# Kernel tuning notes

Measured on AMD Instinct MI355X. Metric: run time of the kernel, lower is better.

The kernel has to match this reference:

```python
import jax, jax.numpy as jnp
import numpy as np
import math

D_MODEL = 1024
NUM_HEADS = 16
D_K = D_MODEL // NUM_HEADS
B, L = 2, 2048


def setup_inputs() -> dict:
    key = jax.random.key(0)
    ks = jax.random.split(key, 9)
    s = 1.0 / math.sqrt(D_MODEL)
    inp = {
        "x": jax.random.normal(ks[0], (B, L, D_MODEL), dtype=jnp.float32),
        "mask": jnp.ones((B, L), dtype=jnp.int32),
        "Wq": jax.random.uniform(ks[1], (D_MODEL, D_MODEL), jnp.float32, -s, s),
        "bq": jax.random.uniform(ks[2], (D_MODEL,), jnp.float32, -s, s),
        "Wk": jax.random.uniform(ks[3], (D_MODEL, D_MODEL), jnp.float32, -s, s),
        "bk": jax.random.uniform(ks[4], (D_MODEL,), jnp.float32, -s, s),
        "Wv": jax.random.uniform(ks[5], (D_MODEL, D_MODEL), jnp.float32, -s, s),
        "bv": jax.random.uniform(ks[6], (D_MODEL,), jnp.float32, -s, s),
        "Wo": jax.random.uniform(ks[7], (D_MODEL, D_MODEL), jnp.float32, -s, s),
        "bo": jax.random.uniform(ks[8], (D_MODEL,), jnp.float32, -s, s),
    }
    return inp


def reference(x, mask, Wq, bq, Wk, bk, Wv, bv, Wo, bo):
    b, l, _ = x.shape
    def proj(W, bias):
        # nn.Linear: x @ W.T + b, then split heads -> [B, H, L, d_k]
        y = x @ W.T + bias
        return y.reshape(b, l, NUM_HEADS, D_K).transpose(0, 2, 1, 3)
    Q, K, V = proj(Wq, bq), proj(Wk, bk), proj(Wv, bv)
    scores = jnp.einsum("bhqd,bhkd->bhqk", Q, K) / math.sqrt(D_K)
    # mask: [B, L] -> [B, 1, 1, L]; fill masked positions with -1e9
    m = mask[:, None, None, :]
    scores = jnp.where(m == 0, jnp.float32(-1e9), scores)
    attn = jax.nn.softmax(scores, axis=-1)
    out = jnp.einsum("bhqk,bhkd->bhqd", attn, V)
    out = out.transpose(0, 2, 1, 3).reshape(b, l, D_MODEL)
    return out @ Wo.T + bo, attn
```

## Files before the change

kernel.cpp:

```cpp
#include <hip/hip_runtime.h>

#define D_MODEL 1024
#define NHEADS  16
#define DKH     64
#define BATCH   2
#define SEQ     2048
#define MTOT    (BATCH*SEQ)
#define NQKV    (3*D_MODEL)
#define LDT     72

typedef __bf16 bf16x8 __attribute__((ext_vector_type(8)));
typedef float  f32x4  __attribute__((ext_vector_type(4)));
typedef unsigned short u16x8 __attribute__((ext_vector_type(8)));
typedef unsigned short u16x4 __attribute__((ext_vector_type(4)));

#define MFMA(a,b,c) __builtin_amdgcn_mfma_f32_16x16x32_bf16(a,b,c,0,0,0)

__device__ __forceinline__ unsigned short f2bf(float f) {
  unsigned u = __builtin_bit_cast(unsigned, f);
  u += 0x7fffu + ((u >> 16) & 1u);
  return (unsigned short)(u >> 16);
}

__device__ __forceinline__ bf16x8 ldfrag(const unsigned short* p) {
  return __builtin_bit_cast(bf16x8, *(const u16x8*)p);
}

__global__ __launch_bounds__(256) void cvt_kernel(const float* __restrict__ src,
                                                  unsigned short* __restrict__ dst, int n4) {
  int i = blockIdx.x * blockDim.x + threadIdx.x;
  if (i >= n4) return;
  float4 f = ((const float4*)src)[i];
  u16x4 o;
  o[0] = f2bf(f.x); o[1] = f2bf(f.y); o[2] = f2bf(f.z); o[3] = f2bf(f.w);
  ((u16x4*)dst)[i] = o;
}

__global__ __launch_bounds__(256) void qkv_gemm(const unsigned short* __restrict__ xbf,
                                                const unsigned short* __restrict__ wbf,
                                                const float* __restrict__ bq,
                                                const float* __restrict__ bk,
                                                const float* __restrict__ bv,
                                                unsigned short* __restrict__ Qo,
                                                unsigned short* __restrict__ Ko,
                                                unsigned short* __restrict__ VTo)
{
  __shared__ __attribute__((aligned(16))) unsigned short As[64*LDT];
  __shared__ __attribute__((aligned(16))) unsigned short Bs[64*LDT];
  const int tid  = threadIdx.x;
  const int wid  = tid >> 6;
  const int lane = tid & 63;
  const int lr   = lane & 15;
  const int lg   = lane >> 4;
  const int m0   = blockIdx.x * 64;
  const int n0   = blockIdx.y * 64;

  f32x4 zero = {0.f, 0.f, 0.f, 0.f};
  f32x4 acc[4];
  acc[0] = zero; acc[1] = zero; acc[2] = zero; acc[3] = zero;

  const int ko = lg * 8;
  for (int kt = 0; kt < D_MODEL/64; ++kt) {
    __syncthreads();
    for (int v = tid; v < 512; v += 256) {
      int row = v >> 3, c8 = (v & 7) * 8;
      *(u16x8*)&As[row*LDT + c8] = *(const u16x8*)&xbf[(size_t)(m0+row)*D_MODEL + kt*64 + c8];
      *(u16x8*)&Bs[row*LDT + c8] = *(const u16x8*)&wbf[(size_t)(n0+row)*D_MODEL + kt*64 + c8];
    }
    __syncthreads();
    bf16x8 a0 = ldfrag(&As[(wid*16+lr)*LDT + ko]);
    bf16x8 a1 = ldfrag(&As[(wid*16+lr)*LDT + 32 + ko]);
#pragma unroll
    for (int ct = 0; ct < 4; ++ct) {
      bf16x8 b0 = ldfrag(&Bs[(ct*16+lr)*LDT + ko]);
      bf16x8 b1 = ldfrag(&Bs[(ct*16+lr)*LDT + 32 + ko]);
      acc[ct] = MFMA(a0, b0, acc[ct]);
      acc[ct] = MFMA(a1, b1, acc[ct]);
    }
  }

  const int proj = n0 >> 10;
  const int rem0 = n0 & 1023;
  const int h    = rem0 >> 6;
  const float* bias = (proj == 0) ? bq : (proj == 1) ? bk : bv;

  if (proj < 2) {
    unsigned short* dst = (proj == 0) ? Qo : Ko;
#pragma unroll
    for (int ct = 0; ct < 4; ++ct) {
      int col = ct*16 + lr;
      float bval = bias[rem0 + col];
#pragma unroll
      for (int r = 0; r < 4; ++r) {
        int m  = m0 + wid*16 + lg*4 + r;
        int b_ = m >> 11, lq = m & (SEQ-1);
        dst[((size_t)((b_*NHEADS + h)*SEQ + lq))*DKH + col] = f2bf(acc[ct][r] + bval);
      }
    }
  } else {
    __syncthreads();
#pragma unroll
    for (int ct = 0; ct < 4; ++ct) {
      int col = ct*16 + lr;
      float bval = bias[rem0 + col];
#pragma unroll
      for (int r = 0; r < 4; ++r) {
        int row = wid*16 + lg*4 + r;
        As[col*LDT + row] = f2bf(acc[ct][r] + bval);
      }
    }
    __syncthreads();
    int b_ = m0 >> 11, lq0 = m0 & (SEQ-1);
    int bh = b_*NHEADS + h;
    for (int v = tid; v < 512; v += 256) {
      int dk = v >> 3, c8 = (v & 7) * 8;
      *(u16x8*)&VTo[((size_t)(bh*DKH + dk))*SEQ + lq0 + c8] = *(const u16x8*)&As[dk*LDT + c8];
    }
  }
}

__global__ __launch_bounds__(256) void attn_kernel(const unsigned short* __restrict__ Qw,
                                                   const unsigned short* __restrict__ Kw,
                                                   const unsigned short* __restrict__ VTw,
                                                   const int* __restrict__ mask,
                                                   float* __restrict__ attn_out,
                                                   unsigned short* __restrict__ OH)
{
  __shared__ __attribute__((aligned(16))) unsigned short Qs[64*LDT];
  __shared__ __attribute__((aligned(16))) unsigned short Ks[64*LDT];
  __shared__ __attribute__((aligned(16))) unsigned short Vs[64*LDT];
  __shared__ __attribute__((aligned(16))) unsigned short Ps[64*LDT];
  __shared__ float invl[64];

  const int tid  = threadIdx.x;
  const int wid  = tid >> 6;
  const int lane = tid & 63;
  const int lr   = lane & 15;
  const int lg   = lane >> 4;
  const int q0   = blockIdx.x * 64;
  const int bh   = blockIdx.y;
  const int b_   = bh >> 4;
  const int h    = bh & 15;

  const unsigned short* Qb = Qw  + (size_t)bh*SEQ*DKH;
  const unsigned short* Kb = Kw  + (size_t)bh*SEQ*DKH;
  const unsigned short* Vb = VTw + (size_t)bh*DKH*SEQ;

  for (int v = tid; v < 512; v += 256) {
    int row = v >> 3, c8 = (v & 7) * 8;
    *(u16x8*)&Qs[row*LDT + c8] = *(const u16x8*)&Qb[(size_t)(q0+row)*DKH + c8];
  }
  __syncthreads();

  const int ko = lg * 8;
  bf16x8 aq0 = ldfrag(&Qs[(wid*16+lr)*LDT + ko]);
  bf16x8 aq1 = ldfrag(&Qs[(wid*16+lr)*LDT + 32 + ko]);

  f32x4 zero = {0.f, 0.f, 0.f, 0.f};
  float lsum[4] = {0.f, 0.f, 0.f, 0.f};

  for (int kt = 0; kt < SEQ/64; ++kt) {
    __syncthreads();
    for (int v = tid; v < 512; v += 256) {
      int row = v >> 3, c8 = (v & 7) * 8;
      *(u16x8*)&Ks[row*LDT + c8] = *(const u16x8*)&Kb[(size_t)(kt*64+row)*DKH + c8];
    }
    __syncthreads();
#pragma unroll
    for (int ct = 0; ct < 4; ++ct) {
      f32x4 acc = zero;
      bf16x8 b0 = ldfrag(&Ks[(ct*16+lr)*LDT + ko]);
      bf16x8 b1 = ldfrag(&Ks[(ct*16+lr)*LDT + 32 + ko]);
      acc = MFMA(aq0, b0, acc);
      acc = MFMA(aq1, b1, acc);
      int kg = kt*64 + ct*16 + lr;
      bool live = mask[b_*SEQ + kg] != 0;
#pragma unroll
      for (int r = 0; r < 4; ++r) {
        float s = live ? acc[r]*0.125f : -1e9f;
        lsum[r] += __expf(s);
      }
    }
  }
#pragma unroll
  for (int r = 0; r < 4; ++r) {
    float s = lsum[r];
    s += __shfl_xor(s, 1); s += __shfl_xor(s, 2);
    s += __shfl_xor(s, 4); s += __shfl_xor(s, 8);
    if (lr == 0) invl[wid*16 + lg*4 + r] = 1.0f / s;
  }
  __syncthreads();

  float il[4];
  {
    int rowb = wid*16 + lg*4;
    il[0] = invl[rowb+0]; il[1] = invl[rowb+1];
    il[2] = invl[rowb+2]; il[3] = invl[rowb+3];
  }

  f32x4 oacc[4];
  oacc[0] = zero; oacc[1] = zero; oacc[2] = zero; oacc[3] = zero;

  for (int kt = 0; kt < SEQ/64; ++kt) {
    __syncthreads();
    for (int v = tid; v < 512; v += 256) {
      int row = v >> 3, c8 = (v & 7) * 8;
      *(u16x8*)&Ks[row*LDT + c8] = *(const u16x8*)&Kb[(size_t)(kt*64+row)*DKH + c8];
      *(u16x8*)&Vs[row*LDT + c8] = *(const u16x8*)&Vb[(size_t)row*SEQ + kt*64 + c8];
    }
    __syncthreads();
#pragma unroll
    for (int ct = 0; ct < 4; ++ct) {
      f32x4 acc = zero;
      bf16x8 b0 = ldfrag(&Ks[(ct*16+lr)*LDT + ko]);
      bf16x8 b1 = ldfrag(&Ks[(ct*16+lr)*LDT + 32 + ko]);
      acc = MFMA(aq0, b0, acc);
      acc = MFMA(aq1, b1, acc);
      int kg = kt*64 + ct*16 + lr;
      bool live = mask[b_*SEQ + kg] != 0;
#pragma unroll
      for (int r = 0; r < 4; ++r) {
        float s = live ? acc[r]*0.125f : -1e9f;
        float p = __expf(s);
        int row = wid*16 + lg*4 + r;
        float a = p * il[r];
        attn_out[(size_t)(bh*SEQ + q0 + row)*SEQ + kg] = a;
        Ps[row*LDT + ct*16 + lr] = f2bf(a);
      }
    }
    __syncthreads();
    bf16x8 pa0 = ldfrag(&Ps[(wid*16+lr)*LDT + ko]);
    bf16x8 pa1 = ldfrag(&Ps[(wid*16+lr)*LDT + 32 + ko]);
#pragma unroll
    for (int ct = 0; ct < 4; ++ct) {
      bf16x8 v0 = ldfrag(&Vs[(ct*16+lr)*LDT + ko]);
      bf16x8 v1 = ldfrag(&Vs[(ct*16+lr)*LDT + 32 + ko]);
      oacc[ct] = MFMA(pa0, v0, oacc[ct]);
      oacc[ct] = MFMA(pa1, v1, oacc[ct]);
    }
  }

#pragma unroll
  for (int ct = 0; ct < 4; ++ct) {
    int dk = ct*16 + lr;
#pragma unroll
    for (int r = 0; r < 4; ++r) {
      int q = q0 + wid*16 + lg*4 + r;
      OH[(size_t)(b_*SEQ + q)*D_MODEL + h*DKH + dk] = f2bf(oacc[ct][r]);
    }
  }
}

__global__ __launch_bounds__(256) void out_gemm(const unsigned short* __restrict__ OH,
                                                const unsigned short* __restrict__ wo,
                                                const float* __restrict__ bo,
                                                float* __restrict__ out)
{
  __shared__ __attribute__((aligned(16))) unsigned short As[64*LDT];
  __shared__ __attribute__((aligned(16))) unsigned short Bs[64*LDT];
  const int tid  = threadIdx.x;
  const int wid  = tid >> 6;
  const int lane = tid & 63;
  const int lr   = lane & 15;
  const int lg   = lane >> 4;
  const int m0   = blockIdx.x * 64;
  const int n0   = blockIdx.y * 64;

  f32x4 zero = {0.f, 0.f, 0.f, 0.f};
  f32x4 acc[4];
  acc[0] = zero; acc[1] = zero; acc[2] = zero; acc[3] = zero;

  const int ko = lg * 8;
  for (int kt = 0; kt < D_MODEL/64; ++kt) {
    __syncthreads();
    for (int v = tid; v < 512; v += 256) {
      int row = v >> 3, c8 = (v & 7) * 8;
      *(u16x8*)&As[row*LDT + c8] = *(const u16x8*)&OH[(size_t)(m0+row)*D_MODEL + kt*64 + c8];
      *(u16x8*)&Bs[row*LDT + c8] = *(const u16x8*)&wo[(size_t)(n0+row)*D_MODEL + kt*64 + c8];
    }
    __syncthreads();
    bf16x8 a0 = ldfrag(&As[(wid*16+lr)*LDT + ko]);
    bf16x8 a1 = ldfrag(&As[(wid*16+lr)*LDT + 32 + ko]);
#pragma unroll
    for (int ct = 0; ct < 4; ++ct) {
      bf16x8 b0 = ldfrag(&Bs[(ct*16+lr)*LDT + ko]);
      bf16x8 b1 = ldfrag(&Bs[(ct*16+lr)*LDT + 32 + ko]);
      acc[ct] = MFMA(a0, b0, acc[ct]);
      acc[ct] = MFMA(a1, b1, acc[ct]);
    }
  }
#pragma unroll
  for (int ct = 0; ct < 4; ++ct) {
    int n = n0 + ct*16 + lr;
    float bval = bo[n];
#pragma unroll
    for (int r = 0; r < 4; ++r) {
      int m = m0 + wid*16 + lg*4 + r;
      out[(size_t)m*D_MODEL + n] = acc[ct][r] + bval;
    }
  }
}

extern "C" void kernel_launch(void* const* d_in, const int* in_sizes, int n_in,
                              void* d_out, int out_size, void* d_ws, size_t ws_size,
                              hipStream_t stream) {
  const float* x    = (const float*)d_in[0];
  const int*   mask = (const int*)  d_in[1];
  const float* Wq   = (const float*)d_in[2];
  const float* bq   = (const float*)d_in[3];
  const float* Wk   = (const float*)d_in[4];
  const float* bk   = (const float*)d_in[5];
  const float* Wv   = (const float*)d_in[6];
  const float* bv   = (const float*)d_in[7];
  const float* Wo   = (const float*)d_in[8];
  const float* bo   = (const float*)d_in[9];

  float* out0 = (float*)d_out;
  float* attn = out0 + (size_t)MTOT * D_MODEL;

  unsigned short* ws   = (unsigned short*)d_ws;
  unsigned short* xbf  = ws;
  unsigned short* wqkv = xbf  + (size_t)MTOT * D_MODEL;
  unsigned short* wob  = wqkv + (size_t)NQKV * D_MODEL;
  unsigned short* Qw   = wob  + (size_t)D_MODEL * D_MODEL;
  unsigned short* Kw   = Qw   + (size_t)MTOT * D_MODEL;
  unsigned short* VTw  = Kw   + (size_t)MTOT * D_MODEL;
  unsigned short* OH   = VTw  + (size_t)MTOT * D_MODEL;

  cvt_kernel<<<4096, 256, 0, stream>>>(x,  xbf, MTOT*D_MODEL/4);
  cvt_kernel<<<1024, 256, 0, stream>>>(Wq, wqkv,                 D_MODEL*D_MODEL/4);
  cvt_kernel<<<1024, 256, 0, stream>>>(Wk, wqkv +   D_MODEL*D_MODEL, D_MODEL*D_MODEL/4);
  cvt_kernel<<<1024, 256, 0, stream>>>(Wv, wqkv + 2*D_MODEL*D_MODEL, D_MODEL*D_MODEL/4);
  cvt_kernel<<<1024, 256, 0, stream>>>(Wo, wob, D_MODEL*D_MODEL/4);

  qkv_gemm<<<dim3(MTOT/64, NQKV/64), 256, 0, stream>>>(xbf, wqkv, bq, bk, bv, Qw, Kw, VTw);
  attn_kernel<<<dim3(SEQ/64, BATCH*NHEADS), 256, 0, stream>>>(Qw, Kw, VTw, mask, attn, OH);
  out_gemm<<<dim3(MTOT/64, D_MODEL/64), 256, 0, stream>>>(OH, wob, bo, out0);
}
```

Before: 821.3 us.

## Transpose score MFMA, drop LDS K/V staging, precompute additive mask, vectorize attn stores

Swaps the MFMA operand order so each lane owns one query row. K, Q and V^T fragments are now loaded straight from global memory instead of being staged in shared memory, which removes all block-wide barriers from both passes. The mask is precomputed once into an additive float buffer placed in the reused x workspace, and the 1/sqrt(dk) scale is folded into an exp2 argument. Attention probabilities are written as non-temporal float4 stores, and P is staged in a per-wave shared tile. The risk is more redundant global and L2 traffic for K/V, since each wave fetches its own fragments with no shared-memory reuse.

```diff
diff --git a/kernel.cpp b/kernel.cpp
--- a/kernel.cpp
+++ b/kernel.cpp
@@ -8,6 +8,7 @@
 #define MTOT    (BATCH*SEQ)
 #define NQKV    (3*D_MODEL)
 #define LDT     72
+#define LDP     72
 
 typedef __bf16 bf16x8 __attribute__((ext_vector_type(8)));
 typedef float  f32x4  __attribute__((ext_vector_type(4)));
@@ -15,6 +16,12 @@
 typedef unsigned short u16x4 __attribute__((ext_vector_type(4)));
 
 #define MFMA(a,b,c) __builtin_amdgcn_mfma_f32_16x16x32_bf16(a,b,c,0,0,0)
+
+#if __has_builtin(__builtin_amdgcn_exp2f)
+#define EXP2(x) __builtin_amdgcn_exp2f(x)
+#else
+#define EXP2(x) exp2f(x)
+#endif
 
 __device__ __forceinline__ unsigned short f2bf(float f) {
   unsigned u = __builtin_bit_cast(unsigned, f);
@@ -34,6 +41,12 @@
   u16x4 o;
   o[0] = f2bf(f.x); o[1] = f2bf(f.y); o[2] = f2bf(f.z); o[3] = f2bf(f.w);
   ((u16x4*)dst)[i] = o;
+}
+
+__global__ __launch_bounds__(256) void mask_kernel(const int* __restrict__ m,
+                                                   float* __restrict__ mf, int n) {
+  int i = blockIdx.x * blockDim.x + threadIdx.x;
+  if (i < n) mf[i] = m[i] ? 0.0f : -1e9f;
 }
 
 __global__ __launch_bounds__(256) void qkv_gemm(const unsigned short* __restrict__ xbf,
@@ -122,15 +135,11 @@
 __global__ __launch_bounds__(256) void attn_kernel(const unsigned short* __restrict__ Qw,
                                                    const unsigned short* __restrict__ Kw,
                                                    const unsigned short* __restrict__ VTw,
-                                                   const int* __restrict__ mask,
+                                                   const float* __restrict__ maskf,
                                                    float* __restrict__ attn_out,
                                                    unsigned short* __restrict__ OH)
 {
-  __shared__ __attribute__((aligned(16))) unsigned short Qs[64*LDT];
-  __shared__ __attribute__((aligned(16))) unsigned short Ks[64*LDT];
-  __shared__ __attribute__((aligned(16))) unsigned short Vs[64*LDT];
-  __shared__ __attribute__((aligned(16))) unsigned short Ps[64*LDT];
-  __shared__ float invl[64];
+  __shared__ __attribute__((aligned(16))) unsigned short Ps[4*16*LDP];
 
   const int tid  = threadIdx.x;
   const int wid  = tid >> 6;
@@ -145,96 +154,71 @@
   const unsigned short* Qb = Qw  + (size_t)bh*SEQ*DKH;
   const unsigned short* Kb = Kw  + (size_t)bh*SEQ*DKH;
   const unsigned short* Vb = VTw + (size_t)bh*DKH*SEQ;
-
-  for (int v = tid; v < 512; v += 256) {
-    int row = v >> 3, c8 = (v & 7) * 8;
-    *(u16x8*)&Qs[row*LDT + c8] = *(const u16x8*)&Qb[(size_t)(q0+row)*DKH + c8];
-  }
-  __syncthreads();
-
-  const int ko = lg * 8;
-  bf16x8 aq0 = ldfrag(&Qs[(wid*16+lr)*LDT + ko]);
-  bf16x8 aq1 = ldfrag(&Qs[(wid*16+lr)*LDT + 32 + ko]);
-
+  const f32x4* mf4 = (const f32x4*)(maskf + b_*SEQ);
+
+  const int qrow = q0 + wid*16 + lr;
+  bf16x8 aq0 = ldfrag(&Qb[(size_t)qrow*DKH + lg*8]);
+  bf16x8 aq1 = ldfrag(&Qb[(size_t)qrow*DKH + 32 + lg*8]);
+
+  const float c2 = 0.18033688011112042f;
   f32x4 zero = {0.f, 0.f, 0.f, 0.f};
-  float lsum[4] = {0.f, 0.f, 0.f, 0.f};
-
+
+  const unsigned short* Kl = Kb + (size_t)lr*DKH + lg*8;
+
+  float lsum = 0.f;
   for (int kt = 0; kt < SEQ/64; ++kt) {
-    __syncthreads();
-    for (int v = tid; v < 512; v += 256) {
-      int row = v >> 3, c8 = (v & 7) * 8;
-      *(u16x8*)&Ks[row*LDT + c8] = *(const u16x8*)&Kb[(size_t)(kt*64+row)*DKH + c8];
-    }
-    __syncthreads();
-#pragma unroll
-    for (int ct = 0; ct < 4; ++ct) {
+    const unsigned short* Kt = Kl + (size_t)kt*64*DKH;
+#pragma unroll
+    for (int ct = 0; ct < 4; ++ct) {
+      bf16x8 k0 = ldfrag(Kt + ct*16*DKH);
+      bf16x8 k1 = ldfrag(Kt + ct*16*DKH + 32);
       f32x4 acc = zero;
-      bf16x8 b0 = ldfrag(&Ks[(ct*16+lr)*LDT + ko]);
-      bf16x8 b1 = ldfrag(&Ks[(ct*16+lr)*LDT + 32 + ko]);
-      acc = MFMA(aq0, b0, acc);
-      acc = MFMA(aq1, b1, acc);
-      int kg = kt*64 + ct*16 + lr;
-      bool live = mask[b_*SEQ + kg] != 0;
-#pragma unroll
-      for (int r = 0; r < 4; ++r) {
-        float s = live ? acc[r]*0.125f : -1e9f;
-        lsum[r] += __expf(s);
-      }
-    }
-  }
-#pragma unroll
-  for (int r = 0; r < 4; ++r) {
-    float s = lsum[r];
-    s += __shfl_xor(s, 1); s += __shfl_xor(s, 2);
-    s += __shfl_xor(s, 4); s += __shfl_xor(s, 8);
-    if (lr == 0) invl[wid*16 + lg*4 + r] = 1.0f / s;
-  }
-  __syncthreads();
-
-  float il[4];
-  {
-    int rowb = wid*16 + lg*4;
-    il[0] = invl[rowb+0]; il[1] = invl[rowb+1];
-    il[2] = invl[rowb+2]; il[3] = invl[rowb+3];
-  }
+      acc = MFMA(k0, aq0, acc);
+      acc = MFMA(k1, aq1, acc);
+      f32x4 md = mf4[kt*16 + ct*4 + lg];
+#pragma unroll
+      for (int r = 0; r < 4; ++r)
+        lsum += EXP2(__builtin_fmaf(acc[r], c2, md[r]));
+    }
+  }
+  lsum += __shfl_xor(lsum, 16);
+  lsum += __shfl_xor(lsum, 32);
+  const float il = 1.0f / lsum;
 
   f32x4 oacc[4];
   oacc[0] = zero; oacc[1] = zero; oacc[2] = zero; oacc[3] = zero;
 
+  unsigned short* PsW = &Ps[wid*16*LDP];
+  float* arow = attn_out + ((size_t)bh*SEQ + qrow)*SEQ;
+  const unsigned short* Vl = Vb + (size_t)lr*SEQ + lg*8;
+
   for (int kt = 0; kt < SEQ/64; ++kt) {
-    __syncthreads();
-    for (int v = tid; v < 512; v += 256) {
-      int row = v >> 3, c8 = (v & 7) * 8;
-      *(u16x8*)&Ks[row*LDT + c8] = *(const u16x8*)&Kb[(size_t)(kt*64+row)*DKH + c8];
-      *(u16x8*)&Vs[row*LDT + c8] = *(const u16x8*)&Vb[(size_t)row*SEQ + kt*64 + c8];
-    }
-    __syncthreads();
-#pragma unroll
-    for (int ct = 0; ct < 4; ++ct) {
+    const unsigned short* Kt = Kl + (size_t)kt*64*DKH;
+#pragma unroll
+    for (int ct = 0; ct < 4; ++ct) {
+      bf16x8 k0 = ldfrag(Kt + ct*16*DKH);
+      bf16x8 k1 = ldfrag(Kt + ct*16*DKH + 32);
       f32x4 acc = zero;
-      bf16x8 b0 = ldfrag(&Ks[(ct*16+lr)*LDT + ko]);
-      bf16x8 b1 = ldfrag(&Ks[(ct*16+lr)*LDT + 32 + ko]);
-      acc = MFMA(aq0, b0, acc);
-      acc = MFMA(aq1, b1, acc);
-      int kg = kt*64 + ct*16 + lr;
-      bool live = mask[b_*SEQ + kg] != 0;
-#pragma unroll
-      for (int r = 0; r < 4; ++r) {
-        float s = live ? acc[r]*0.125f : -1e9f;
-        float p = __expf(s);
-        int row = wid*16 + lg*4 + r;
-        float a = p * il[r];
-        attn_out[(size_t)(bh*SEQ + q0 + row)*SEQ + kg] = a;
-        Ps[row*LDT + ct*16 + lr] = f2bf(a);
-      }
-    }
-    __syncthreads();
-    bf16x8 pa0 = ldfrag(&Ps[(wid*16+lr)*LDT + ko]);
-    bf16x8 pa1 = ldfrag(&Ps[(wid*16+lr)*LDT + 32 + ko]);
-#pragma unroll
-    for (int ct = 0; ct < 4; ++ct) {
-      bf16x8 v0 = ldfrag(&Vs[(ct*16+lr)*LDT + ko]);
-      bf16x8 v1 = ldfrag(&Vs[(ct*16+lr)*LDT + 32 + ko]);
+      acc = MFMA(k0, aq0, acc);
+      acc = MFMA(k1, aq1, acc);
+      f32x4 md = mf4[kt*16 + ct*4 + lg];
+      f32x4 av;
+#pragma unroll
+      for (int r = 0; r < 4; ++r)
+        av[r] = EXP2(__builtin_fmaf(acc[r], c2, md[r])) * il;
+      __builtin_nontemporal_store(av, (f32x4*)(arow + kt*64 + ct*16 + lg*4));
+      u16x4 pk;
+      pk[0] = f2bf(av[0]); pk[1] = f2bf(av[1]);
+      pk[2] = f2bf(av[2]); pk[3] = f2bf(av[3]);
+      *(u16x4*)&PsW[lr*LDP + ct*16 + lg*4] = pk;
+    }
+    bf16x8 pa0 = ldfrag(&PsW[lr*LDP + lg*8]);
+    bf16x8 pa1 = ldfrag(&PsW[lr*LDP + 32 + lg*8]);
+    const unsigned short* Vt = Vl + kt*64;
+#pragma unroll
+    for (int ct = 0; ct < 4; ++ct) {
+      bf16x8 v0 = ldfrag(Vt + (size_t)ct*16*SEQ);
+      bf16x8 v1 = ldfrag(Vt + (size_t)ct*16*SEQ + 32);
       oacc[ct] = MFMA(pa0, v0, oacc[ct]);
       oacc[ct] = MFMA(pa1, v1, oacc[ct]);
     }
@@ -327,6 +311,8 @@
   unsigned short* VTw  = Kw   + (size_t)MTOT * D_MODEL;
   unsigned short* OH   = VTw  + (size_t)MTOT * D_MODEL;
 
+  float* maskf = (float*)xbf;
+
   cvt_kernel<<<4096, 256, 0, stream>>>(x,  xbf, MTOT*D_MODEL/4);
   cvt_kernel<<<1024, 256, 0, stream>>>(Wq, wqkv,                 D_MODEL*D_MODEL/4);
   cvt_kernel<<<1024, 256, 0, stream>>>(Wk, wqkv +   D_MODEL*D_MODEL, D_MODEL*D_MODEL/4);
@@ -334,6 +320,7 @@
   cvt_kernel<<<1024, 256, 0, stream>>>(Wo, wob, D_MODEL*D_MODEL/4);
 
   qkv_gemm<<<dim3(MTOT/64, NQKV/64), 256, 0, stream>>>(xbf, wqkv, bq, bk, bv, Qw, Kw, VTw);
-  attn_kernel<<<dim3(SEQ/64, BATCH*NHEADS), 256, 0, stream>>>(Qw, Kw, VTw, mask, attn, OH);
+  mask_kernel<<<16, 256, 0, stream>>>(mask, maskf, BATCH*SEQ);
+  attn_kernel<<<dim3(SEQ/64, BATCH*NHEADS), 256, 0, stream>>>(Qw, Kw, VTw, maskf, attn, OH);
   out_gemm<<<dim3(MTOT/64, D_MODEL/64), 256, 0, stream>>>(OH, wob, bo, out0);
 }
```

Result: slower. 939.1 us (+14.3%).
